# Optimization experiments

Hardware: AMD Instinct MI355X
Metric: run time of the kernel (lower is better)

## Reference

```python
import jax, jax.numpy as jnp
from jax import lax
import numpy as np

B, N, WID = 4096, 16, 64


def setup_inputs() -> dict:
    key = jax.random.key(0)
    ks = jax.random.split(key, 10)
    def nrm(k, shape, fan):
        return (jax.random.normal(k, shape) / np.float32(np.sqrt(fan))).astype(jnp.float32)
    x = 2.0 * jax.random.randint(ks[0], (B, N, N), 0, 2).astype(jnp.float32) - 1.0  # spins +/-1
    return {
        "x": x,
        "Wx": nrm(ks[1], (1, 2), 2),          # intermediate_x: Linear(2,1,bias=False)
        "Wh": nrm(ks[2], (WID, 2 * WID), 2 * WID),   # intermediate_h
        "Wh2": nrm(ks[3], (WID, 2 * WID), 2 * WID),  # intermediate_h2
        "Wih": nrm(ks[4], (4 * WID, 2), 2),   # LSTMCell weight_ih
        "Whh": nrm(ks[5], (4 * WID, WID), WID),  # LSTMCell weight_hh
        "bih": nrm(ks[6], (4 * WID,), WID),
        "bhh": nrm(ks[7], (4 * WID,), WID),
        "Wfc": nrm(ks[8], (2, WID), WID),     # fc1
        "bfc": nrm(ks[9], (2,), WID),
    }


def _log_prob(x, Wx, Wh, Wh2, Wih, Whh, bih, bhh, Wfc, bfc):
    Bn, n, _ = x.shape
    Wd = Whh.shape[1]
    dt = x.dtype

    # zigzag traversal: even rows left->right, odd rows right->left.
    # perm maps traversal position t -> column index; involutive (identity or reversal).
    perms = jnp.stack([jnp.arange(n) if i % 2 == 0 else jnp.arange(n)[::-1]
                       for i in range(n)])  # [n, n]
    x_rows = jnp.transpose(x, (1, 0, 2))                                  # [n, B, n]
    x_up_rows = jnp.concatenate([jnp.zeros((1, Bn, n), dt), x_rows[:-1]], 0)  # [n, B, n]

    Wh_p, Wh_u = Wh[:, :Wd], Wh[:, Wd:]
    Wh2_p, Wh2_u = Wh2[:, :Wd], Wh2[:, Wd:]

    def cell(carry, xs):
        h_prev, c_prev = carry          # [B, W] each (in-row previous cell, zeros at row start)
        x_prev, x_up, h_up, c_up = xs   # [B], [B], [B,W], [B,W]
        # slot 1 = previous cell along traversal, slot 2 = cell above
        x_inter = x_prev * Wx[0, 0] + x_up * Wx[0, 1]                     # [B]
        h_inter = h_prev @ Wh_p.T + h_up @ Wh_u.T                          # [B, W]
        c_inter = c_prev @ Wh2_p.T + c_up @ Wh2_u.T                        # [B, W]
        xh = (x_inter + 1.0) * 0.5
        emb = jnp.stack([xh, 1.0 - xh], axis=-1)                           # [B, 2]
        gates = emb @ Wih.T + bih + h_inter @ Whh.T + bhh                  # [B, 4W]
        ig, fg, gg, og = jnp.split(gates, 4, axis=-1)
        c_new = jax.nn.sigmoid(fg) * c_inter + jax.nn.sigmoid(ig) * jnp.tanh(gg)
        h_new = jax.nn.sigmoid(og) * jnp.tanh(c_new)
        y = jax.nn.log_softmax(h_new @ Wfc.T + bfc, axis=-1)               # [B, 2]
        return (h_new, c_new), (h_new, c_new, y)

    def row_step(carry, xs):
        h_row, c_row = carry            # [B, n, W] states of previous row (column order)
        x_row, x_up_row, perm = xs
        x_trav = x_row[:, perm]                                            # [B, n]
        x_prev_trav = jnp.concatenate([jnp.zeros((Bn, 1), dt), x_trav[:, :-1]], 1)
        x_up_trav = x_up_row[:, perm]
        h_up_trav = jnp.transpose(h_row[:, perm], (1, 0, 2))               # [n, B, W]
        c_up_trav = jnp.transpose(c_row[:, perm], (1, 0, 2))
        init = (jnp.zeros((Bn, Wd), dt), jnp.zeros((Bn, Wd), dt))
        _, (h_t, c_t, y_t) = lax.scan(
            cell, init, (x_prev_trav.T, x_up_trav.T, h_up_trav, c_up_trav))
        # traversal order -> column order (perm is its own inverse)
        h_col = jnp.transpose(h_t[perm], (1, 0, 2))                        # [B, n, W]
        c_col = jnp.transpose(c_t[perm], (1, 0, 2))
        y_col = y_t[perm]                                                  # [n, B, 2]
        return (h_col, c_col), y_col

    init = (jnp.zeros((Bn, n, Wd), dt), jnp.zeros((Bn, n, Wd), dt))
    _, ys = lax.scan(row_step, init, (x_rows, x_up_rows, perms))           # [n, n, B, 2]
    y = jnp.transpose(ys, (2, 0, 1, 3))                                    # [B, n, n, 2]

    mask = (1.0 + x) * 0.5
    lp = y[..., 0] * mask + y[..., 1] * (1.0 - mask)                       # [B, n, n]
    # final correction: samples with exactly one up spin
    aa = mask.sum((1, 2))
    rec = aa == 1
    jc = 0 if n % 2 == 0 else n - 1  # last visited cell of the zigzag
    factor = jnp.where(rec, 1.0 - mask[:, n - 1, jc], jnp.ones((), dt))
    lp = lp.at[:, n - 1, jc].multiply(factor)
    return lp.sum((1, 2))


def reference(x, Wx, Wh, Wh2, Wih, Whh, bih, bhh, Wfc, bfc):
    return _log_prob(x, Wx, Wh, Wh2, Wih, Whh, bih, bhh, Wfc, bfc)
```

## Files before the change

### kernel.cpp

```cpp
#include <hip/hip_runtime.h>

typedef __bf16 bf16x8 __attribute__((ext_vector_type(8)));
typedef float f32x4 __attribute__((ext_vector_type(4)));

#define MFMA(a,b,c) __builtin_amdgcn_mfma_f32_16x16x32_bf16((a),(b),(c),0,0,0)

__device__ __forceinline__ float rcp_(float x){ return __builtin_amdgcn_rcpf(x); }

__global__ __launch_bounds__(256) void prep_kernel(
    const float* __restrict__ Wh,  const float* __restrict__ Wh2,
    const float* __restrict__ Whh, const float* __restrict__ Wfc,
    __bf16* __restrict__ tbl)
{
  const int idx = blockIdx.x*256 + threadIdx.x;
  if (idx >= 256*176) return;
  const int e = idx & 7, f = (idx >> 3) % 22, t = idx / 176;
  const int w = t >> 6, lane = t & 63, l16 = lane & 15, g8 = (lane >> 4) * 8;
  float val;
  if (f < 16){
    const int g = (f >> 1) & 3, s = f & 1, half = f >> 3;
    const int n = g*64 + w*16 + l16;
    const int k = s*32 + g8 + e;
    const float* whcol = Wh + half*64 + k;
    float acc = 0.f;
    for (int j=0; j<64; ++j) acc += Whh[n*64 + j] * whcol[j*128];
    val = (g == 2) ? 2.f*acc : acc;
  } else if (f < 20){
    const int s = f - 16;
    const int n = w*16 + l16;
    const int k = s*32 + g8 + e;
    val = Wh2[n*128 + k];
  } else {
    const int s = f - 20;
    const int k = s*32 + g8 + e;
    val = Wfc[k] - Wfc[64 + k];
  }
  tbl[t*176 + f*8 + e] = (__bf16)val;
}

__global__ __launch_bounds__(256,1) void lstm2d_kernel(
    const float* __restrict__ x,   const float* __restrict__ Wx,
    const float* __restrict__ Wih,
    const float* __restrict__ bih, const float* __restrict__ bhh,
    const float* __restrict__ bfc,
    const __bf16* __restrict__ tbl,
    float* __restrict__ out)
{
  __shared__ __align__(16) __bf16 s_h[16*16*64];
  __shared__ __align__(16) __bf16 s_c[16*16*64];
  __shared__ __align__(16) float  s_xh[256*16];
  __shared__ unsigned int s_msk[16*8];

  const int tid  = threadIdx.x;
  const int w    = tid >> 6;
  const int lane = tid & 63;
  const int l16  = lane & 15;
  const int g4   = lane >> 4;
  const int g8   = g4 * 8;

  const float wx0 = Wx[0], wx1 = Wx[1];

  unsigned int* zh = (unsigned int*)s_h;
  unsigned int* zc = (unsigned int*)s_c;
  #pragma unroll
  for (int it=0; it<32; ++it){ zh[tid + it*256] = 0u; zc[tid + it*256] = 0u; }

  const float* xg = x + blockIdx.x * 4096;
  #pragma unroll
  for (int k=0; k<16; ++k){
    const int idx = tid + k*256;
    const int row = idx & 15, slot = idx >> 4;
    const int i = slot >> 4, t = slot & 15;
    const int c   = (i & 1) ? 15 - t : t;
    const int cpc = (i & 1) ? c + 1 : c - 1;
    const float xp = (t > 0) ? xg[row*256 + i*16 + cpc] : 0.f;
    const float xu = (i > 0) ? xg[row*256 + (i-1)*16 + c] : 0.f;
    s_xh[slot*16 + row] = (xp*wx0 + xu*wx1 + 1.f) * 0.5f;
  }
  if (tid < 128){
    const int row = tid >> 3, wd = tid & 7;
    unsigned int m = 0;
    for (int b=0; b<32; ++b){
      const int slot = wd*32 + b, i = slot >> 4, t = slot & 15;
      const int c = (i & 1) ? 15 - t : t;
      if (xg[row*256 + i*16 + c] > 0.f) m |= (1u << b);
    }
    s_msk[row*8 + wd] = m;
  }

  const __bf16* tb = tbl + tid*176;
  bf16x8 G1f[4][2], G2f[4][2], bcf[4], fcB[2];
  #pragma unroll
  for (int g=0; g<4; ++g)
    #pragma unroll
    for (int s=0; s<2; ++s){
      G1f[g][s] = *(const bf16x8*)(tb + (g*2+s)*8);
      G2f[g][s] = *(const bf16x8*)(tb + 64 + (g*2+s)*8);
    }
  #pragma unroll
  for (int s=0; s<4; ++s) bcf[s] = *(const bf16x8*)(tb + 128 + s*8);
  #pragma unroll
  for (int s=0; s<2; ++s) fcB[s] = *(const bf16x8*)(tb + 160 + s*8);

  const float bd = bfc[0] - bfc[1];
  float base_[4], dvec_[4];
  #pragma unroll
  for (int g=0; g<4; ++g){
    const int cg = g*64 + w*16 + l16;
    const float sc = (g == 2) ? 2.f : 1.f;
    base_[g] = (bih[cg] + bhh[cg] + Wih[cg*2+1]) * sc;
    dvec_[g] = (Wih[cg*2+0] - Wih[cg*2+1]) * sc;
  }
  const int colw = w*16 + l16;

  const int offA0 = l16*64 + ((     g8) ^ ((l16 & 7) << 3));
  const int offA1 = l16*64 + ((32 + g8) ^ ((l16 & 7) << 3));
  int stW[4];
  #pragma unroll
  for (int r=0;r<4;++r){
    const int row = g4*4 + r;
    stW[r] = row*64 + (colw ^ ((row & 7) << 3));
  }

  float lp[4] = {0.f,0.f,0.f,0.f};
  int   aa[4] = {0,0,0,0};

  __syncthreads();

  f32x4 accGu[4], aCu, aFp;

  for (int i=0; i<16; ++i){
    const int dir = i & 1;
    const int slot0 = i*16;

    {
      const int b = (dir ? 15 : 0) << 10;
      bf16x8 ah0 = *(const bf16x8*)(s_h + b + offA0);
      bf16x8 ah1 = *(const bf16x8*)(s_h + b + offA1);
      bf16x8 qc0 = *(const bf16x8*)(s_c + b + offA0);
      bf16x8 qc1 = *(const bf16x8*)(s_c + b + offA1);
      const float4 xh4 = *(const float4*)(s_xh + slot0*16 + g4*4);
      #pragma unroll
      for (int g=0; g<4; ++g){
        accGu[g][0] = base_[g] + xh4.x * dvec_[g];
        accGu[g][1] = base_[g] + xh4.y * dvec_[g];
        accGu[g][2] = base_[g] + xh4.z * dvec_[g];
        accGu[g][3] = base_[g] + xh4.w * dvec_[g];
        accGu[g] = MFMA(ah0, G2f[g][0], accGu[g]);
        accGu[g] = MFMA(ah1, G2f[g][1], accGu[g]);
      }
      f32x4 z = {0.f,0.f,0.f,0.f};
      aCu = MFMA(qc0, bcf[2], z);
      aCu = MFMA(qc1, bcf[3], aCu);
      f32x4 fz = {bd,bd,bd,bd};
      fz = MFMA(ah0, fcB[0], fz);
      aFp = MFMA(ah1, fcB[1], fz);
    }

    for (int t=0; t<16; ++t){
      const int c    = dir ? 15 - t : t;
      const int slot = slot0 + t;

      f32x4 accG[4], aC, aF;
      if (t > 0){
        const int b = (dir ? c + 1 : c - 1) << 10;
        bf16x8 a0 = *(const bf16x8*)(s_h + b + offA0);
        bf16x8 a1 = *(const bf16x8*)(s_h + b + offA1);
        bf16x8 q0 = *(const bf16x8*)(s_c + b + offA0);
        bf16x8 q1 = *(const bf16x8*)(s_c + b + offA1);
        #pragma unroll
        for (int g=0; g<4; ++g){
          accG[g] = MFMA(a0, G1f[g][0], accGu[g]);
          accG[g] = MFMA(a1, G1f[g][1], accG[g]);
        }
        aC = MFMA(q0, bcf[0], aCu);
        aC = MFMA(q1, bcf[1], aC);
        f32x4 fz = {bd,bd,bd,bd};
        fz = MFMA(a0, fcB[0], fz);
        aF = MFMA(a1, fcB[1], fz);
      } else {
        #pragma unroll
        for (int g=0; g<4; ++g) accG[g] = accGu[g];
        aC = aCu; aF = aFp;
      }

      if (slot > 0){
        const int ps = slot - 1;
        #pragma unroll
        for (int r=0;r<4;++r){
          const int msk = (s_msk[(g4*4+r)*8 + (ps >> 5)] >> (ps & 31)) & 1;
          const float d = aF[r];
          const float zz = msk ? -d : d;
          lp[r] -= __logf(1.f + __expf(zz));
          aa[r] += msk;
        }
      }

      if (t < 15){
        const int bu = (dir ? 14 - t : t + 1) << 10;
        bf16x8 au0 = *(const bf16x8*)(s_h + bu + offA0);
        bf16x8 au1 = *(const bf16x8*)(s_h + bu + offA1);
        bf16x8 cu0 = *(const bf16x8*)(s_c + bu + offA0);
        bf16x8 cu1 = *(const bf16x8*)(s_c + bu + offA1);
        const float4 xh4 = *(const float4*)(s_xh + (slot+1)*16 + g4*4);
        #pragma unroll
        for (int g=0; g<4; ++g){
          accGu[g][0] = base_[g] + xh4.x * dvec_[g];
          accGu[g][1] = base_[g] + xh4.y * dvec_[g];
          accGu[g][2] = base_[g] + xh4.z * dvec_[g];
          accGu[g][3] = base_[g] + xh4.w * dvec_[g];
          accGu[g] = MFMA(au0, G2f[g][0], accGu[g]);
          accGu[g] = MFMA(au1, G2f[g][1], accGu[g]);
        }
        f32x4 z = {0.f,0.f,0.f,0.f};
        aCu = MFMA(cu0, bcf[2], z);
        aCu = MFMA(cu1, bcf[3], aCu);
      }

      const int cb = c << 10;
      #pragma unroll
      for (int r=0;r<4;++r){
        const float ig = accG[0][r], fg = accG[1][r], gg = accG[2][r], og = accG[3][r];
        const float si = rcp_(1.f + __expf(-ig));
        const float sf = rcp_(1.f + __expf(-fg));
        const float tg = 2.f * rcp_(1.f + __expf(-gg)) - 1.f;
        const float cn = sf * aC[r] + si * tg;
        const float so = rcp_(1.f + __expf(-og));
        const float tc = 2.f * rcp_(1.f + __expf(-2.f*cn)) - 1.f;
        const float hn = so * tc;
        s_h[cb + stW[r]] = (__bf16)hn;
        s_c[cb + stW[r]] = (__bf16)cn;
      }

      __syncthreads();
    }
  }

  {
    bf16x8 a0 = *(const bf16x8*)(s_h + offA0);
    bf16x8 a1 = *(const bf16x8*)(s_h + offA1);
    f32x4 fz = {bd,bd,bd,bd};
    fz = MFMA(a0, fcB[0], fz);
    f32x4 aF = MFMA(a1, fcB[1], fz);
    #pragma unroll
    for (int r=0;r<4;++r){
      const int msk = (s_msk[(g4*4+r)*8 + 7] >> 31) & 1;
      const float d = aF[r];
      const float zz = msk ? -d : d;
      const float contrib = -__logf(1.f + __expf(zz));
      lp[r] += contrib; aa[r] += msk;
      if (aa[r] == 1 && msk) lp[r] -= contrib;
    }
    if (w == 0 && l16 == 0){
      #pragma unroll
      for (int r=0;r<4;++r) out[blockIdx.x*16 + g4*4 + r] = lp[r];
    }
  }
}

extern "C" void kernel_launch(void* const* d_in, const int* in_sizes, int n_in,
                              void* d_out, int out_size, void* d_ws, size_t ws_size,
                              hipStream_t stream) {
  const float* x   = (const float*)d_in[0];
  const float* Wx  = (const float*)d_in[1];
  const float* Wh  = (const float*)d_in[2];
  const float* Wh2 = (const float*)d_in[3];
  const float* Wih = (const float*)d_in[4];
  const float* Whh = (const float*)d_in[5];
  const float* bih = (const float*)d_in[6];
  const float* bhh = (const float*)d_in[7];
  const float* Wfc = (const float*)d_in[8];
  const float* bfc = (const float*)d_in[9];
  float* out = (float*)d_out;
  __bf16* tbl = (__bf16*)d_ws;

  prep_kernel<<<dim3(176), dim3(256), 0, stream>>>(Wh, Wh2, Whh, Wfc, tbl);
  lstm2d_kernel<<<dim3(256), dim3(256), 0, stream>>>(
      x, Wx, Wih, bih, bhh, bfc, tbl, out);
}
```

Baseline: 258.5 us.

## Split LSTM gate work across 8 waves with shuffle exchange and deferred log-prob

Doubles the block to 512 threads so each wave owns 8 hidden columns and computes two gate tiles (half the MFMAs per wave), exchanging gate values between lane halves via shuffles. Folds the log2(e) scaling into the weight tables so exp2f replaces expf, and moves bias/input-weight constants into the prep table. The fc1 logit is computed only by wave 0 and stored to shared memory, and the log-sigmoid reduction is deferred to a parallel pass after the recurrence instead of running every step. The cost is more waves synchronizing at each of the 256 barriers, plus shuffle overhead and an extra reduction phase.

```diff
diff --git a/kernel.cpp b/kernel.cpp
--- a/kernel.cpp
+++ b/kernel.cpp
@@ -6,50 +6,69 @@
 #define MFMA(a,b,c) __builtin_amdgcn_mfma_f32_16x16x32_bf16((a),(b),(c),0,0,0)
 
 __device__ __forceinline__ float rcp_(float x){ return __builtin_amdgcn_rcpf(x); }
+
+#define L2E 1.4426950408889634f
+#define LN2 0.6931471805599453f
 
 __global__ __launch_bounds__(256) void prep_kernel(
     const float* __restrict__ Wh,  const float* __restrict__ Wh2,
     const float* __restrict__ Whh, const float* __restrict__ Wfc,
-    __bf16* __restrict__ tbl)
+    const float* __restrict__ Wih, const float* __restrict__ bih,
+    const float* __restrict__ bhh,
+    char* __restrict__ tblc)
 {
   const int idx = blockIdx.x*256 + threadIdx.x;
-  if (idx >= 256*176) return;
-  const int e = idx & 7, f = (idx >> 3) % 22, t = idx / 176;
-  const int w = t >> 6, lane = t & 63, l16 = lane & 15, g8 = (lane >> 4) * 8;
-  float val;
-  if (f < 16){
-    const int g = (f >> 1) & 3, s = f & 1, half = f >> 3;
-    const int n = g*64 + w*16 + l16;
-    const int k = s*32 + g8 + e;
-    const float* whcol = Wh + half*64 + k;
-    float acc = 0.f;
-    for (int j=0; j<64; ++j) acc += Whh[n*64 + j] * whcol[j*128];
-    val = (g == 2) ? 2.f*acc : acc;
-  } else if (f < 20){
-    const int s = f - 16;
-    const int n = w*16 + l16;
-    const int k = s*32 + g8 + e;
-    val = Wh2[n*128 + k];
-  } else {
-    const int s = f - 20;
-    const int k = s*32 + g8 + e;
-    val = Wfc[k] - Wfc[64 + k];
-  }
-  tbl[t*176 + f*8 + e] = (__bf16)val;
+  if (idx < 512*14*8){
+    const int e = idx & 7, f = (idx >> 3) % 14, t = (idx >> 3) / 14;
+    const int w = t >> 6, lane = t & 63, l16 = lane & 15;
+    const int g8 = ((lane >> 4) & 3) * 8;
+    const int hcol = w*8 + (l16 & 7), hi = l16 >> 3;
+    float val;
+    if (f < 8){
+      const int half = (f >> 2) & 1;
+      const int tile = (f >> 1) & 1;
+      const int s    = f & 1;
+      const int gate = tile*2 + hi;
+      const int n = gate*64 + hcol;
+      const int k = s*32 + g8 + e;
+      float acc = 0.f;
+      for (int j=0; j<64; ++j) acc += Whh[n*64 + j] * Wh[j*128 + half*64 + k];
+      val = acc * ((gate == 2) ? 2.f*L2E : L2E);
+    } else if (f < 12){
+      const int s = f - 8;
+      const int k = (s & 1)*32 + g8 + e;
+      val = Wh2[hcol*128 + (s >> 1)*64 + k];
+    } else {
+      const int k = (f & 1)*32 + g8 + e;
+      val = Wfc[k] - Wfc[64 + k];
+    }
+    *(__bf16*)(tblc + t*240 + f*16 + e*2) = (__bf16)val;
+  } else if (idx < 512*14*8 + 512*4){
+    const int j = idx - 512*14*8;
+    const int t = j >> 2, q = j & 3;
+    const int w = t >> 6, lane = t & 63, l16 = lane & 15, hi = l16 >> 3;
+    const int tile = q >> 1, kind = q & 1;
+    const int gate = tile*2 + hi;
+    const int n = gate*64 + w*8 + (l16 & 7);
+    const float sc = (gate == 2) ? 2.f*L2E : L2E;
+    const float v = kind ? sc*(Wih[n*2] - Wih[n*2+1])
+                         : sc*(bih[n] + bhh[n] + Wih[n*2+1]);
+    *(float*)(tblc + t*240 + 224 + q*4) = v;
+  }
 }
 
-__global__ __launch_bounds__(256,1) void lstm2d_kernel(
+__global__ __launch_bounds__(512,2) void lstm2d_kernel(
     const float* __restrict__ x,   const float* __restrict__ Wx,
-    const float* __restrict__ Wih,
-    const float* __restrict__ bih, const float* __restrict__ bhh,
     const float* __restrict__ bfc,
-    const __bf16* __restrict__ tbl,
+    const char* __restrict__ tblc,
     float* __restrict__ out)
 {
   __shared__ __align__(16) __bf16 s_h[16*16*64];
   __shared__ __align__(16) __bf16 s_c[16*16*64];
   __shared__ __align__(16) float  s_xh[256*16];
+  __shared__ __align__(16) float  s_d[256*16];
   __shared__ unsigned int s_msk[16*8];
+  __shared__ float s_red[8*16];
 
   const int tid  = threadIdx.x;
   const int w    = tid >> 6;
@@ -57,18 +76,21 @@
   const int l16  = lane & 15;
   const int g4   = lane >> 4;
   const int g8   = g4 * 8;
+  const int hi   = l16 >> 3;
+  const bool lo  = (hi == 0);
 
   const float wx0 = Wx[0], wx1 = Wx[1];
+  const float bd  = bfc[0] - bfc[1];
 
   unsigned int* zh = (unsigned int*)s_h;
   unsigned int* zc = (unsigned int*)s_c;
   #pragma unroll
-  for (int it=0; it<32; ++it){ zh[tid + it*256] = 0u; zc[tid + it*256] = 0u; }
+  for (int it=0; it<16; ++it){ zh[tid + it*512] = 0u; zc[tid + it*512] = 0u; }
 
   const float* xg = x + blockIdx.x * 4096;
   #pragma unroll
-  for (int k=0; k<16; ++k){
-    const int idx = tid + k*256;
+  for (int k=0; k<8; ++k){
+    const int idx = tid + k*512;
     const int row = idx & 15, slot = idx >> 4;
     const int i = slot >> 4, t = slot & 15;
     const int c   = (i & 1) ? 15 - t : t;
@@ -88,173 +110,183 @@
     s_msk[row*8 + wd] = m;
   }
 
-  const __bf16* tb = tbl + tid*176;
-  bf16x8 G1f[4][2], G2f[4][2], bcf[4], fcB[2];
+  const char* tb = tblc + tid*240;
+  bf16x8 g1T0[2], g1T1[2], g2T0[2], g2T1[2], cB[4], fcB[2];
+  g1T0[0] = *(const bf16x8*)(tb +   0); g1T0[1] = *(const bf16x8*)(tb +  16);
+  g1T1[0] = *(const bf16x8*)(tb +  32); g1T1[1] = *(const bf16x8*)(tb +  48);
+  g2T0[0] = *(const bf16x8*)(tb +  64); g2T0[1] = *(const bf16x8*)(tb +  80);
+  g2T1[0] = *(const bf16x8*)(tb +  96); g2T1[1] = *(const bf16x8*)(tb + 112);
   #pragma unroll
-  for (int g=0; g<4; ++g)
-    #pragma unroll
-    for (int s=0; s<2; ++s){
-      G1f[g][s] = *(const bf16x8*)(tb + (g*2+s)*8);
-      G2f[g][s] = *(const bf16x8*)(tb + 64 + (g*2+s)*8);
-    }
-  #pragma unroll
-  for (int s=0; s<4; ++s) bcf[s] = *(const bf16x8*)(tb + 128 + s*8);
-  #pragma unroll
-  for (int s=0; s<2; ++s) fcB[s] = *(const bf16x8*)(tb + 160 + s*8);
-
-  const float bd = bfc[0] - bfc[1];
-  float base_[4], dvec_[4];
-  #pragma unroll
-  for (int g=0; g<4; ++g){
-    const int cg = g*64 + w*16 + l16;
-    const float sc = (g == 2) ? 2.f : 1.f;
-    base_[g] = (bih[cg] + bhh[cg] + Wih[cg*2+1]) * sc;
-    dvec_[g] = (Wih[cg*2+0] - Wih[cg*2+1]) * sc;
-  }
-  const int colw = w*16 + l16;
+  for (int s=0; s<4; ++s) cB[s] = *(const bf16x8*)(tb + 128 + s*16);
+  fcB[0] = *(const bf16x8*)(tb + 192); fcB[1] = *(const bf16x8*)(tb + 208);
+  const float base0 = *(const float*)(tb + 224);
+  const float dvec0 = *(const float*)(tb + 228);
+  const float base1 = *(const float*)(tb + 232);
+  const float dvec1 = *(const float*)(tb + 236);
 
   const int offA0 = l16*64 + ((     g8) ^ ((l16 & 7) << 3));
   const int offA1 = l16*64 + ((32 + g8) ^ ((l16 & 7) << 3));
-  int stW[4];
+  const int habs = w*8 + (l16 & 7);
+  int stWa[2];
   #pragma unroll
-  for (int r=0;r<4;++r){
-    const int row = g4*4 + r;
-    stW[r] = row*64 + (colw ^ ((row & 7) << 3));
-  }
-
-  float lp[4] = {0.f,0.f,0.f,0.f};
-  int   aa[4] = {0,0,0,0};
+  for (int e=0; e<2; ++e){
+    const int R = g4*4 + 2*hi + e;
+    stWa[e] = R*64 + (habs ^ ((R & 7) << 3));
+  }
+  const float C2 = -2.f*L2E;
 
   __syncthreads();
 
-  f32x4 accGu[4], aCu, aFp;
+  f32x4 aT0u, aT1u, aCu;
 
   for (int i=0; i<16; ++i){
     const int dir = i & 1;
     const int slot0 = i*16;
 
     {
-      const int b = (dir ? 15 : 0) << 10;
-      bf16x8 ah0 = *(const bf16x8*)(s_h + b + offA0);
-      bf16x8 ah1 = *(const bf16x8*)(s_h + b + offA1);
-      bf16x8 qc0 = *(const bf16x8*)(s_c + b + offA0);
-      bf16x8 qc1 = *(const bf16x8*)(s_c + b + offA1);
+      const int bu = (dir ? 15 : 0) << 10;
+      bf16x8 h0 = *(const bf16x8*)(s_h + bu + offA0);
+      bf16x8 h1 = *(const bf16x8*)(s_h + bu + offA1);
+      bf16x8 c0 = *(const bf16x8*)(s_c + bu + offA0);
+      bf16x8 c1 = *(const bf16x8*)(s_c + bu + offA1);
       const float4 xh4 = *(const float4*)(s_xh + slot0*16 + g4*4);
       #pragma unroll
-      for (int g=0; g<4; ++g){
-        accGu[g][0] = base_[g] + xh4.x * dvec_[g];
-        accGu[g][1] = base_[g] + xh4.y * dvec_[g];
-        accGu[g][2] = base_[g] + xh4.z * dvec_[g];
-        accGu[g][3] = base_[g] + xh4.w * dvec_[g];
-        accGu[g] = MFMA(ah0, G2f[g][0], accGu[g]);
-        accGu[g] = MFMA(ah1, G2f[g][1], accGu[g]);
-      }
+      for (int r=0;r<4;++r){
+        const float xh = (&xh4.x)[r];
+        aT0u[r] = base0 + xh*dvec0;
+        aT1u[r] = base1 + xh*dvec1;
+      }
+      aT0u = MFMA(h0, g2T0[0], aT0u); aT0u = MFMA(h1, g2T0[1], aT0u);
+      aT1u = MFMA(h0, g2T1[0], aT1u); aT1u = MFMA(h1, g2T1[1], aT1u);
       f32x4 z = {0.f,0.f,0.f,0.f};
-      aCu = MFMA(qc0, bcf[2], z);
-      aCu = MFMA(qc1, bcf[3], aCu);
-      f32x4 fz = {bd,bd,bd,bd};
-      fz = MFMA(ah0, fcB[0], fz);
-      aFp = MFMA(ah1, fcB[1], fz);
+      aCu = MFMA(c0, cB[2], z); aCu = MFMA(c1, cB[3], aCu);
+      if (w == 0 && i > 0){
+        f32x4 fz = {bd,bd,bd,bd};
+        fz = MFMA(h0, fcB[0], fz);
+        f32x4 aF = MFMA(h1, fcB[1], fz);
+        if (l16 == 0){
+          #pragma unroll
+          for (int r=0;r<4;++r) s_d[(slot0-1)*16 + g4*4 + r] = aF[r];
+        }
+      }
     }
 
     for (int t=0; t<16; ++t){
       const int c    = dir ? 15 - t : t;
       const int slot = slot0 + t;
 
-      f32x4 accG[4], aC, aF;
+      f32x4 aT0 = aT0u, aT1 = aT1u, aC = aCu;
       if (t > 0){
-        const int b = (dir ? c + 1 : c - 1) << 10;
-        bf16x8 a0 = *(const bf16x8*)(s_h + b + offA0);
-        bf16x8 a1 = *(const bf16x8*)(s_h + b + offA1);
-        bf16x8 q0 = *(const bf16x8*)(s_c + b + offA0);
-        bf16x8 q1 = *(const bf16x8*)(s_c + b + offA1);
-        #pragma unroll
-        for (int g=0; g<4; ++g){
-          accG[g] = MFMA(a0, G1f[g][0], accGu[g]);
-          accG[g] = MFMA(a1, G1f[g][1], accG[g]);
+        const int bp = (dir ? c + 1 : c - 1) << 10;
+        bf16x8 a0 = *(const bf16x8*)(s_h + bp + offA0);
+        bf16x8 a1 = *(const bf16x8*)(s_h + bp + offA1);
+        bf16x8 q0 = *(const bf16x8*)(s_c + bp + offA0);
+        bf16x8 q1 = *(const bf16x8*)(s_c + bp + offA1);
+        aT0 = MFMA(a0, g1T0[0], aT0); aT0 = MFMA(a1, g1T0[1], aT0);
+        aT1 = MFMA(a0, g1T1[0], aT1); aT1 = MFMA(a1, g1T1[1], aT1);
+        aC  = MFMA(q0, cB[0], aC);    aC  = MFMA(q1, cB[1], aC);
+        if (w == 0){
+          f32x4 fz = {bd,bd,bd,bd};
+          fz = MFMA(a0, fcB[0], fz);
+          f32x4 aF = MFMA(a1, fcB[1], fz);
+          if (l16 == 0){
+            #pragma unroll
+            for (int r=0;r<4;++r) s_d[(slot-1)*16 + g4*4 + r] = aF[r];
+          }
         }
-        aC = MFMA(q0, bcf[0], aCu);
-        aC = MFMA(q1, bcf[1], aC);
-        f32x4 fz = {bd,bd,bd,bd};
-        fz = MFMA(a0, fcB[0], fz);
-        aF = MFMA(a1, fcB[1], fz);
-      } else {
-        #pragma unroll
-        for (int g=0; g<4; ++g) accG[g] = accGu[g];
-        aC = aCu; aF = aFp;
-      }
-
-      if (slot > 0){
-        const int ps = slot - 1;
+      }
+
+      if (t < 15){
+        const int bu = (dir ? 14 - t : t + 1) << 10;
+        bf16x8 h0 = *(const bf16x8*)(s_h + bu + offA0);
+        bf16x8 h1 = *(const bf16x8*)(s_h + bu + offA1);
+        bf16x8 c0 = *(const bf16x8*)(s_c + bu + offA0);
+        bf16x8 c1 = *(const bf16x8*)(s_c + bu + offA1);
+        const float4 xh4 = *(const float4*)(s_xh + (slot+1)*16 + g4*4);
         #pragma unroll
         for (int r=0;r<4;++r){
-          const int msk = (s_msk[(g4*4+r)*8 + (ps >> 5)] >> (ps & 31)) & 1;
-          const float d = aF[r];
-          const float zz = msk ? -d : d;
-          lp[r] -= __logf(1.f + __expf(zz));
-          aa[r] += msk;
+          const float xh = (&xh4.x)[r];
+          aT0u[r] = base0 + xh*dvec0;
+          aT1u[r] = base1 + xh*dvec1;
         }
-      }
-
-      if (t < 15){
-        const int bu = (dir ? 14 - t : t + 1) << 10;
-        bf16x8 au0 = *(const bf16x8*)(s_h + bu + offA0);
-        bf16x8 au1 = *(const bf16x8*)(s_h + bu + offA1);
-        bf16x8 cu0 = *(const bf16x8*)(s_c + bu + offA0);
-        bf16x8 cu1 = *(const bf16x8*)(s_c + bu + offA1);
-        const float4 xh4 = *(const float4*)(s_xh + (slot+1)*16 + g4*4);
-        #pragma unroll
-        for (int g=0; g<4; ++g){
-          accGu[g][0] = base_[g] + xh4.x * dvec_[g];
-          accGu[g][1] = base_[g] + xh4.y * dvec_[g];
-          accGu[g][2] = base_[g] + xh4.z * dvec_[g];
-          accGu[g][3] = base_[g] + xh4.w * dvec_[g];
-          accGu[g] = MFMA(au0, G2f[g][0], accGu[g]);
-          accGu[g] = MFMA(au1, G2f[g][1], accGu[g]);
-        }
+        aT0u = MFMA(h0, g2T0[0], aT0u); aT0u = MFMA(h1, g2T0[1], aT0u);
+        aT1u = MFMA(h0, g2T1[0], aT1u); aT1u = MFMA(h1, g2T1[1], aT1u);
         f32x4 z = {0.f,0.f,0.f,0.f};
-        aCu = MFMA(cu0, bcf[2], z);
-        aCu = MFMA(cu1, bcf[3], aCu);
+        aCu = MFMA(c0, cB[2], z); aCu = MFMA(c1, cB[3], aCu);
       }
 
       const int cb = c << 10;
       #pragma unroll
-      for (int r=0;r<4;++r){
-        const float ig = accG[0][r], fg = accG[1][r], gg = accG[2][r], og = accG[3][r];
-        const float si = rcp_(1.f + __expf(-ig));
-        const float sf = rcp_(1.f + __expf(-fg));
-        const float tg = 2.f * rcp_(1.f + __expf(-gg)) - 1.f;
-        const float cn = sf * aC[r] + si * tg;
-        const float so = rcp_(1.f + __expf(-og));
-        const float tc = 2.f * rcp_(1.f + __expf(-2.f*cn)) - 1.f;
+      for (int e=0; e<2; ++e){
+        const float sendT0 = lo ? aT0[2+e] : aT0[e];
+        const float sendT1 = lo ? aT1[2+e] : aT1[e];
+        const float rT0 = __shfl_xor(sendT0, 8);
+        const float rT1 = __shfl_xor(sendT1, 8);
+        const float own0 = lo ? aT0[e] : aT0[2+e];
+        const float own1 = lo ? aT1[e] : aT1[2+e];
+        const float ig = lo ? own0 : rT0;
+        const float fg = lo ? rT0  : own0;
+        const float gg = lo ? own1 : rT1;
+        const float og = lo ? rT1  : own1;
+        const float cI = lo ? aC[e] : aC[2+e];
+        const float si = rcp_(1.f + exp2f(-ig));
+        const float sf = rcp_(1.f + exp2f(-fg));
+        const float tg = 2.f * rcp_(1.f + exp2f(-gg)) - 1.f;
+        const float cn = sf*cI + si*tg;
+        const float so = rcp_(1.f + exp2f(-og));
+        const float tc = 2.f * rcp_(1.f + exp2f(C2*cn)) - 1.f;
         const float hn = so * tc;
-        s_h[cb + stW[r]] = (__bf16)hn;
-        s_c[cb + stW[r]] = (__bf16)cn;
+        s_h[cb + stWa[e]] = (__bf16)hn;
+        s_c[cb + stWa[e]] = (__bf16)cn;
       }
 
       __syncthreads();
     }
   }
 
-  {
+  if (w == 0){
     bf16x8 a0 = *(const bf16x8*)(s_h + offA0);
     bf16x8 a1 = *(const bf16x8*)(s_h + offA1);
     f32x4 fz = {bd,bd,bd,bd};
     fz = MFMA(a0, fcB[0], fz);
     f32x4 aF = MFMA(a1, fcB[1], fz);
+    if (l16 == 0){
+      #pragma unroll
+      for (int r=0;r<4;++r) s_d[255*16 + g4*4 + r] = aF[r];
+    }
+  }
+  __syncthreads();
+
+  {
+    const int row = tid & 15, grp = tid >> 4;
+    float lpp = 0.f;
     #pragma unroll
-    for (int r=0;r<4;++r){
-      const int msk = (s_msk[(g4*4+r)*8 + 7] >> 31) & 1;
-      const float d = aF[r];
+    for (int e=0; e<8; ++e){
+      const int slot = grp*8 + e;
+      const float d = s_d[slot*16 + row];
+      const int msk = (s_msk[row*8 + (slot >> 5)] >> (slot & 31)) & 1;
       const float zz = msk ? -d : d;
-      const float contrib = -__logf(1.f + __expf(zz));
-      lp[r] += contrib; aa[r] += msk;
-      if (aa[r] == 1 && msk) lp[r] -= contrib;
-    }
-    if (w == 0 && l16 == 0){
-      #pragma unroll
-      for (int r=0;r<4;++r) out[blockIdx.x*16 + g4*4 + r] = lp[r];
-    }
+      lpp -= LN2 * log2f(1.f + exp2f(zz * L2E));
+    }
+    lpp += __shfl_xor(lpp, 16);
+    lpp += __shfl_xor(lpp, 32);
+    if (lane < 16) s_red[w*16 + lane] = lpp;
+  }
+  __syncthreads();
+  if (tid < 16){
+    const int row = tid;
+    float lp = 0.f;
+    #pragma unroll
+    for (int ww=0; ww<8; ++ww) lp += s_red[ww*16 + row];
+    int aa = 0;
+    #pragma unroll
+    for (int wd=0; wd<8; ++wd) aa += __popc(s_msk[row*8 + wd]);
+    const int m255 = (s_msk[row*8 + 7] >> 31) & 1;
+    if (aa == 1 && m255){
+      const float d = s_d[255*16 + row];
+      lp += LN2 * log2f(1.f + exp2f(-d * L2E));
+    }
+    out[blockIdx.x*16 + row] = lp;
   }
 }
 
@@ -272,9 +304,9 @@
   const float* Wfc = (const float*)d_in[8];
   const float* bfc = (const float*)d_in[9];
   float* out = (float*)d_out;
-  __bf16* tbl = (__bf16*)d_ws;
-
-  prep_kernel<<<dim3(176), dim3(256), 0, stream>>>(Wh, Wh2, Whh, Wfc, tbl);
-  lstm2d_kernel<<<dim3(256), dim3(256), 0, stream>>>(
-      x, Wx, Wih, bih, bhh, bfc, tbl, out);
+  char* tbl = (char*)d_ws;
+
+  prep_kernel<<<dim3(((512*14*8 + 512*4) + 255)/256), dim3(256), 0, stream>>>(
+      Wh, Wh2, Whh, Wfc, Wih, bih, bhh, tbl);
+  lstm2d_kernel<<<dim3(256), dim3(512), 0, stream>>>(x, Wx, bfc, tbl, out);
 }
```

Result: slower. 274.4 us (+6.1%).

## Halve samples per block to 8 and defer log-prob reduction to epilogue

Applied to the files above, without the earlier changes.

Each block now handles 8 samples instead of 16, so the grid doubles to 512 blocks and spreads work over more compute units on the serial 256-step recurrence. The MFMA M-dimension is still 16, so half the rows are duplicated and only lanes with g4<2 store results, which wastes half of each MFMA. The fc logit is computed by a single rotating wave per step and stored to shared memory. The softplus log-prob accumulation moves out of the recurrent loop into a parallel reduction at the end.

```diff
diff --git a/kernel.cpp b/kernel.cpp
--- a/kernel.cpp
+++ b/kernel.cpp
@@ -46,10 +46,12 @@
     const __bf16* __restrict__ tbl,
     float* __restrict__ out)
 {
-  __shared__ __align__(16) __bf16 s_h[16*16*64];
-  __shared__ __align__(16) __bf16 s_c[16*16*64];
-  __shared__ __align__(16) float  s_xh[256*16];
-  __shared__ unsigned int s_msk[16*8];
+  __shared__ __align__(16) __bf16 s_h[16*8*64];
+  __shared__ __align__(16) __bf16 s_c[16*8*64];
+  __shared__ __align__(16) float  s_xh[256*8];
+  __shared__ __align__(16) float  s_d[256*8];
+  __shared__ unsigned int s_msk[8*8];
+  __shared__ float s_red[32];
 
   const int tid  = threadIdx.x;
   const int w    = tid >> 6;
@@ -57,27 +59,29 @@
   const int l16  = lane & 15;
   const int g4   = lane >> 4;
   const int g8   = g4 * 8;
+  const int rl   = l16 & 7;
+  const bool vld = (g4 < 2);
 
   const float wx0 = Wx[0], wx1 = Wx[1];
 
   unsigned int* zh = (unsigned int*)s_h;
   unsigned int* zc = (unsigned int*)s_c;
   #pragma unroll
-  for (int it=0; it<32; ++it){ zh[tid + it*256] = 0u; zc[tid + it*256] = 0u; }
-
-  const float* xg = x + blockIdx.x * 4096;
-  #pragma unroll
-  for (int k=0; k<16; ++k){
+  for (int it=0; it<16; ++it){ zh[tid + it*256] = 0u; zc[tid + it*256] = 0u; }
+
+  const float* xg = x + blockIdx.x * 2048;
+  #pragma unroll
+  for (int k=0; k<8; ++k){
     const int idx = tid + k*256;
-    const int row = idx & 15, slot = idx >> 4;
+    const int row = idx & 7, slot = idx >> 3;
     const int i = slot >> 4, t = slot & 15;
     const int c   = (i & 1) ? 15 - t : t;
     const int cpc = (i & 1) ? c + 1 : c - 1;
     const float xp = (t > 0) ? xg[row*256 + i*16 + cpc] : 0.f;
     const float xu = (i > 0) ? xg[row*256 + (i-1)*16 + c] : 0.f;
-    s_xh[slot*16 + row] = (xp*wx0 + xu*wx1 + 1.f) * 0.5f;
-  }
-  if (tid < 128){
+    s_xh[slot*8 + row] = (xp*wx0 + xu*wx1 + 1.f) * 0.5f;
+  }
+  if (tid < 64){
     const int row = tid >> 3, wd = tid & 7;
     unsigned int m = 0;
     for (int b=0; b<32; ++b){
@@ -113,33 +117,31 @@
   }
   const int colw = w*16 + l16;
 
-  const int offA0 = l16*64 + ((     g8) ^ ((l16 & 7) << 3));
-  const int offA1 = l16*64 + ((32 + g8) ^ ((l16 & 7) << 3));
+  const int offA0 = rl*64 + ((     g8) ^ (rl << 3));
+  const int offA1 = rl*64 + ((32 + g8) ^ (rl << 3));
   int stW[4];
   #pragma unroll
   for (int r=0;r<4;++r){
-    const int row = g4*4 + r;
-    stW[r] = row*64 + (colw ^ ((row & 7) << 3));
-  }
-
-  float lp[4] = {0.f,0.f,0.f,0.f};
-  int   aa[4] = {0,0,0,0};
+    const int R = (g4 & 1)*4 + r;
+    stW[r] = R*64 + (colw ^ (R << 3));
+  }
+  const int xhOff = (g4 & 1) * 4;
 
   __syncthreads();
 
-  f32x4 accGu[4], aCu, aFp;
+  f32x4 accGu[4], aCu;
 
   for (int i=0; i<16; ++i){
     const int dir = i & 1;
     const int slot0 = i*16;
 
     {
-      const int b = (dir ? 15 : 0) << 10;
+      const int b = (dir ? 15 : 0) << 9;
       bf16x8 ah0 = *(const bf16x8*)(s_h + b + offA0);
       bf16x8 ah1 = *(const bf16x8*)(s_h + b + offA1);
       bf16x8 qc0 = *(const bf16x8*)(s_c + b + offA0);
       bf16x8 qc1 = *(const bf16x8*)(s_c + b + offA1);
-      const float4 xh4 = *(const float4*)(s_xh + slot0*16 + g4*4);
+      const float4 xh4 = *(const float4*)(s_xh + slot0*8 + xhOff);
       #pragma unroll
       for (int g=0; g<4; ++g){
         accGu[g][0] = base_[g] + xh4.x * dvec_[g];
@@ -152,18 +154,24 @@
       f32x4 z = {0.f,0.f,0.f,0.f};
       aCu = MFMA(qc0, bcf[2], z);
       aCu = MFMA(qc1, bcf[3], aCu);
-      f32x4 fz = {bd,bd,bd,bd};
-      fz = MFMA(ah0, fcB[0], fz);
-      aFp = MFMA(ah1, fcB[1], fz);
+      if (i > 0 && w == 3){
+        f32x4 fz = {bd,bd,bd,bd};
+        fz = MFMA(ah0, fcB[0], fz);
+        f32x4 aF = MFMA(ah1, fcB[1], fz);
+        if (l16 == 0 && vld){
+          #pragma unroll
+          for (int r=0;r<4;++r) s_d[(slot0-1)*8 + (g4&1)*4 + r] = aF[r];
+        }
+      }
     }
 
     for (int t=0; t<16; ++t){
       const int c    = dir ? 15 - t : t;
       const int slot = slot0 + t;
 
-      f32x4 accG[4], aC, aF;
+      f32x4 accG[4], aC;
       if (t > 0){
-        const int b = (dir ? c + 1 : c - 1) << 10;
+        const int b = (dir ? c + 1 : c - 1) << 9;
         bf16x8 a0 = *(const bf16x8*)(s_h + b + offA0);
         bf16x8 a1 = *(const bf16x8*)(s_h + b + offA1);
         bf16x8 q0 = *(const bf16x8*)(s_c + b + offA0);
@@ -175,34 +183,28 @@
         }
         aC = MFMA(q0, bcf[0], aCu);
         aC = MFMA(q1, bcf[1], aC);
-        f32x4 fz = {bd,bd,bd,bd};
-        fz = MFMA(a0, fcB[0], fz);
-        aF = MFMA(a1, fcB[1], fz);
+        if (w == ((t - 1) & 3)){
+          f32x4 fz = {bd,bd,bd,bd};
+          fz = MFMA(a0, fcB[0], fz);
+          f32x4 aF = MFMA(a1, fcB[1], fz);
+          if (l16 == 0 && vld){
+            #pragma unroll
+            for (int r=0;r<4;++r) s_d[(slot-1)*8 + (g4&1)*4 + r] = aF[r];
+          }
+        }
       } else {
         #pragma unroll
         for (int g=0; g<4; ++g) accG[g] = accGu[g];
-        aC = aCu; aF = aFp;
-      }
-
-      if (slot > 0){
-        const int ps = slot - 1;
-        #pragma unroll
-        for (int r=0;r<4;++r){
-          const int msk = (s_msk[(g4*4+r)*8 + (ps >> 5)] >> (ps & 31)) & 1;
-          const float d = aF[r];
-          const float zz = msk ? -d : d;
-          lp[r] -= __logf(1.f + __expf(zz));
-          aa[r] += msk;
-        }
+        aC = aCu;
       }
 
       if (t < 15){
-        const int bu = (dir ? 14 - t : t + 1) << 10;
+        const int bu = (dir ? 14 - t : t + 1) << 9;
         bf16x8 au0 = *(const bf16x8*)(s_h + bu + offA0);
         bf16x8 au1 = *(const bf16x8*)(s_h + bu + offA1);
         bf16x8 cu0 = *(const bf16x8*)(s_c + bu + offA0);
         bf16x8 cu1 = *(const bf16x8*)(s_c + bu + offA1);
-        const float4 xh4 = *(const float4*)(s_xh + (slot+1)*16 + g4*4);
+        const float4 xh4 = *(const float4*)(s_xh + (slot+1)*8 + xhOff);
         #pragma unroll
         for (int g=0; g<4; ++g){
           accGu[g][0] = base_[g] + xh4.x * dvec_[g];
@@ -217,44 +219,71 @@
         aCu = MFMA(cu1, bcf[3], aCu);
       }
 
-      const int cb = c << 10;
-      #pragma unroll
-      for (int r=0;r<4;++r){
-        const float ig = accG[0][r], fg = accG[1][r], gg = accG[2][r], og = accG[3][r];
-        const float si = rcp_(1.f + __expf(-ig));
-        const float sf = rcp_(1.f + __expf(-fg));
-        const float tg = 2.f * rcp_(1.f + __expf(-gg)) - 1.f;
-        const float cn = sf * aC[r] + si * tg;
-        const float so = rcp_(1.f + __expf(-og));
-        const float tc = 2.f * rcp_(1.f + __expf(-2.f*cn)) - 1.f;
-        const float hn = so * tc;
-        s_h[cb + stW[r]] = (__bf16)hn;
-        s_c[cb + stW[r]] = (__bf16)cn;
+      if (vld){
+        const int cb = c << 9;
+        #pragma unroll
+        for (int r=0;r<4;++r){
+          const float ig = accG[0][r], fg = accG[1][r], gg = accG[2][r], og = accG[3][r];
+          const float si = rcp_(1.f + __expf(-ig));
+          const float sf = rcp_(1.f + __expf(-fg));
+          const float tg = 2.f * rcp_(1.f + __expf(-gg)) - 1.f;
+          const float cn = sf * aC[r] + si * tg;
+          const float so = rcp_(1.f + __expf(-og));
+          const float tc = 2.f * rcp_(1.f + __expf(-2.f*cn)) - 1.f;
+          const float hn = so * tc;
+          s_h[cb + stW[r]] = (__bf16)hn;
+          s_c[cb + stW[r]] = (__bf16)cn;
+        }
       }
 
       __syncthreads();
     }
   }
 
-  {
+  if (w == 3){
     bf16x8 a0 = *(const bf16x8*)(s_h + offA0);
     bf16x8 a1 = *(const bf16x8*)(s_h + offA1);
     f32x4 fz = {bd,bd,bd,bd};
     fz = MFMA(a0, fcB[0], fz);
     f32x4 aF = MFMA(a1, fcB[1], fz);
+    if (l16 == 0 && vld){
+      #pragma unroll
+      for (int r=0;r<4;++r) s_d[255*8 + (g4&1)*4 + r] = aF[r];
+    }
+  }
+  __syncthreads();
+
+  {
+    const int row = lane & 7, grpw = lane >> 3;
+    float lpp = 0.f;
     #pragma unroll
-    for (int r=0;r<4;++r){
-      const int msk = (s_msk[(g4*4+r)*8 + 7] >> 31) & 1;
-      const float d = aF[r];
+    for (int e=0; e<8; ++e){
+      const int slot = (w*8 + grpw)*8 + e;
+      const float d = s_d[slot*8 + row];
+      const int msk = (s_msk[row*8 + (slot >> 5)] >> (slot & 31)) & 1;
       const float zz = msk ? -d : d;
-      const float contrib = -__logf(1.f + __expf(zz));
-      lp[r] += contrib; aa[r] += msk;
-      if (aa[r] == 1 && msk) lp[r] -= contrib;
-    }
-    if (w == 0 && l16 == 0){
-      #pragma unroll
-      for (int r=0;r<4;++r) out[blockIdx.x*16 + g4*4 + r] = lp[r];
-    }
+      lpp -= __logf(1.f + __expf(zz));
+    }
+    lpp += __shfl_xor(lpp, 8);
+    lpp += __shfl_xor(lpp, 16);
+    lpp += __shfl_xor(lpp, 32);
+    if (lane < 8) s_red[w*8 + lane] = lpp;
+  }
+  __syncthreads();
+  if (tid < 8){
+    const int row = tid;
+    float lp = 0.f;
+    #pragma unroll
+    for (int ww=0; ww<4; ++ww) lp += s_red[ww*8 + row];
+    int aa = 0;
+    #pragma unroll
+    for (int wd=0; wd<8; ++wd) aa += __popc(s_msk[row*8 + wd]);
+    const int m255 = (s_msk[row*8 + 7] >> 31) & 1;
+    if (aa == 1 && m255){
+      const float d = s_d[255*8 + row];
+      lp += __logf(1.f + __expf(-d));
+    }
+    out[blockIdx.x*8 + row] = lp;
   }
 }
 
@@ -275,6 +304,6 @@
   __bf16* tbl = (__bf16*)d_ws;
 
   prep_kernel<<<dim3(176), dim3(256), 0, stream>>>(Wh, Wh2, Whh, Wfc, tbl);
-  lstm2d_kernel<<<dim3(256), dim3(256), 0, stream>>>(
+  lstm2d_kernel<<<dim3(512), dim3(256), 0, stream>>>(
       x, Wx, Wih, bih, bhh, bfc, tbl, out);
 }
```

Measured after the change: 300.7 us. +16.3%, slower.

## Defer log-prob to an epilogue, round-robin fc1 across waves, fold log2e into weights

Applied to the files above, without the earlier changes.

The fc1 projection is now computed by a single wave per step, chosen round-robin. The per-slot logit is stored in shared memory, and all softplus log-prob terms plus the up-spin count are evaluated in a parallel epilogue after the recurrence. This takes them off the serial per-cell critical path. The gate weights and biases are prescaled by log2(e) so the LSTM activations use exp2. The sigmoid/tanh combination is also rewritten to share reciprocals, cutting the transcendental count per cell. The cost is extra LDS (s_d, s_red) and a final reduction pass.

```diff
diff --git a/kernel.cpp b/kernel.cpp
--- a/kernel.cpp
+++ b/kernel.cpp
@@ -6,6 +6,8 @@
 #define MFMA(a,b,c) __builtin_amdgcn_mfma_f32_16x16x32_bf16((a),(b),(c),0,0,0)
 
 __device__ __forceinline__ float rcp_(float x){ return __builtin_amdgcn_rcpf(x); }
+
+#define L2E 1.4426950408889634f
 
 __global__ __launch_bounds__(256) void prep_kernel(
     const float* __restrict__ Wh,  const float* __restrict__ Wh2,
@@ -24,7 +26,7 @@
     const float* whcol = Wh + half*64 + k;
     float acc = 0.f;
     for (int j=0; j<64; ++j) acc += Whh[n*64 + j] * whcol[j*128];
-    val = (g == 2) ? 2.f*acc : acc;
+    val = acc * ((g == 2) ? 2.f*L2E : L2E);
   } else if (f < 20){
     const int s = f - 16;
     const int n = w*16 + l16;
@@ -49,7 +51,9 @@
   __shared__ __align__(16) __bf16 s_h[16*16*64];
   __shared__ __align__(16) __bf16 s_c[16*16*64];
   __shared__ __align__(16) float  s_xh[256*16];
+  __shared__ __align__(16) float  s_d[256*16];
   __shared__ unsigned int s_msk[16*8];
+  __shared__ float s_red[256];
 
   const int tid  = threadIdx.x;
   const int w    = tid >> 6;
@@ -107,7 +111,7 @@
   #pragma unroll
   for (int g=0; g<4; ++g){
     const int cg = g*64 + w*16 + l16;
-    const float sc = (g == 2) ? 2.f : 1.f;
+    const float sc = (g == 2) ? 2.f*L2E : L2E;
     base_[g] = (bih[cg] + bhh[cg] + Wih[cg*2+1]) * sc;
     dvec_[g] = (Wih[cg*2+0] - Wih[cg*2+1]) * sc;
   }
@@ -121,13 +125,11 @@
     const int row = g4*4 + r;
     stW[r] = row*64 + (colw ^ ((row & 7) << 3));
   }
-
-  float lp[4] = {0.f,0.f,0.f,0.f};
-  int   aa[4] = {0,0,0,0};
+  const float C2 = -2.f*L2E;
 
   __syncthreads();
 
-  f32x4 accGu[4], aCu, aFp;
+  f32x4 accGu[4], aCu;
 
   for (int i=0; i<16; ++i){
     const int dir = i & 1;
@@ -152,16 +154,22 @@
       f32x4 z = {0.f,0.f,0.f,0.f};
       aCu = MFMA(qc0, bcf[2], z);
       aCu = MFMA(qc1, bcf[3], aCu);
-      f32x4 fz = {bd,bd,bd,bd};
-      fz = MFMA(ah0, fcB[0], fz);
-      aFp = MFMA(ah1, fcB[1], fz);
+      if (i > 0 && w == 3){
+        f32x4 fz = {bd,bd,bd,bd};
+        fz = MFMA(ah0, fcB[0], fz);
+        f32x4 aF = MFMA(ah1, fcB[1], fz);
+        if (l16 == 0){
+          #pragma unroll
+          for (int r=0;r<4;++r) s_d[(slot0-1)*16 + g4*4 + r] = aF[r];
+        }
+      }
     }
 
     for (int t=0; t<16; ++t){
       const int c    = dir ? 15 - t : t;
       const int slot = slot0 + t;
 
-      f32x4 accG[4], aC, aF;
+      f32x4 accG[4], aC;
       if (t > 0){
         const int b = (dir ? c + 1 : c - 1) << 10;
         bf16x8 a0 = *(const bf16x8*)(s_h + b + offA0);
@@ -175,25 +183,19 @@
         }
         aC = MFMA(q0, bcf[0], aCu);
         aC = MFMA(q1, bcf[1], aC);
-        f32x4 fz = {bd,bd,bd,bd};
-        fz = MFMA(a0, fcB[0], fz);
-        aF = MFMA(a1, fcB[1], fz);
+        if (w == ((t - 1) & 3)){
+          f32x4 fz = {bd,bd,bd,bd};
+          fz = MFMA(a0, fcB[0], fz);
+          f32x4 aF = MFMA(a1, fcB[1], fz);
+          if (l16 == 0){
+            #pragma unroll
+            for (int r=0;r<4;++r) s_d[(slot-1)*16 + g4*4 + r] = aF[r];
+          }
+        }
       } else {
         #pragma unroll
         for (int g=0; g<4; ++g) accG[g] = accGu[g];
-        aC = aCu; aF = aFp;
-      }
-
-      if (slot > 0){
-        const int ps = slot - 1;
-        #pragma unroll
-        for (int r=0;r<4;++r){
-          const int msk = (s_msk[(g4*4+r)*8 + (ps >> 5)] >> (ps & 31)) & 1;
-          const float d = aF[r];
-          const float zz = msk ? -d : d;
-          lp[r] -= __logf(1.f + __expf(zz));
-          aa[r] += msk;
-        }
+        aC = aCu;
       }
 
       if (t < 15){
@@ -217,44 +219,70 @@
         aCu = MFMA(cu1, bcf[3], aCu);
       }
 
-      const int cb = c << 10;
-      #pragma unroll
-      for (int r=0;r<4;++r){
-        const float ig = accG[0][r], fg = accG[1][r], gg = accG[2][r], og = accG[3][r];
-        const float si = rcp_(1.f + __expf(-ig));
-        const float sf = rcp_(1.f + __expf(-fg));
-        const float tg = 2.f * rcp_(1.f + __expf(-gg)) - 1.f;
-        const float cn = sf * aC[r] + si * tg;
-        const float so = rcp_(1.f + __expf(-og));
-        const float tc = 2.f * rcp_(1.f + __expf(-2.f*cn)) - 1.f;
-        const float hn = so * tc;
-        s_h[cb + stW[r]] = (__bf16)hn;
-        s_c[cb + stW[r]] = (__bf16)cn;
+      {
+        const int cb = c << 10;
+        #pragma unroll
+        for (int r=0;r<4;++r){
+          const float A = exp2f(-accG[0][r]);
+          const float F = exp2f(-accG[1][r]);
+          const float B = exp2f(-accG[2][r]);
+          const float O = exp2f(-accG[3][r]);
+          const float a1 = 1.f + A, f1 = 1.f + F, b1 = 1.f + B, o1 = 1.f + O;
+          const float pab = a1 * b1;
+          const float num = fmaf(1.f - B, f1, aC[r] * pab);
+          const float cn  = num * rcp_(pab * f1);
+          const float E   = exp2f(C2 * cn);
+          const float hn  = (1.f - E) * rcp_(o1 * (1.f + E));
+          s_h[cb + stW[r]] = (__bf16)hn;
+          s_c[cb + stW[r]] = (__bf16)cn;
+        }
       }
 
       __syncthreads();
     }
   }
 
-  {
+  if (w == 3){
     bf16x8 a0 = *(const bf16x8*)(s_h + offA0);
     bf16x8 a1 = *(const bf16x8*)(s_h + offA1);
     f32x4 fz = {bd,bd,bd,bd};
     fz = MFMA(a0, fcB[0], fz);
     f32x4 aF = MFMA(a1, fcB[1], fz);
+    if (l16 == 0){
+      #pragma unroll
+      for (int r=0;r<4;++r) s_d[255*16 + g4*4 + r] = aF[r];
+    }
+  }
+  __syncthreads();
+
+  {
+    const int row = tid & 15, grp = tid >> 4;
+    float lpp = 0.f;
     #pragma unroll
-    for (int r=0;r<4;++r){
-      const int msk = (s_msk[(g4*4+r)*8 + 7] >> 31) & 1;
-      const float d = aF[r];
+    for (int e=0; e<16; ++e){
+      const int slot = grp*16 + e;
+      const float d = s_d[slot*16 + row];
+      const int msk = (s_msk[row*8 + (slot >> 5)] >> (slot & 31)) & 1;
       const float zz = msk ? -d : d;
-      const float contrib = -__logf(1.f + __expf(zz));
-      lp[r] += contrib; aa[r] += msk;
-      if (aa[r] == 1 && msk) lp[r] -= contrib;
-    }
-    if (w == 0 && l16 == 0){
-      #pragma unroll
-      for (int r=0;r<4;++r) out[blockIdx.x*16 + g4*4 + r] = lp[r];
-    }
+      lpp -= __logf(1.f + __expf(zz));
+    }
+    s_red[grp*16 + row] = lpp;
+  }
+  __syncthreads();
+  if (tid < 16){
+    const int row = tid;
+    float lp = 0.f;
+    #pragma unroll
+    for (int g=0; g<16; ++g) lp += s_red[g*16 + row];
+    int aa = 0;
+    #pragma unroll
+    for (int wd=0; wd<8; ++wd) aa += __popc(s_msk[row*8 + wd]);
+    const int m255 = (s_msk[row*8 + 7] >> 31) & 1;
+    if (aa == 1 && m255){
+      const float d = s_d[255*16 + row];
+      lp += __logf(1.f + __expf(-d));
+    }
+    out[blockIdx.x*16 + row] = lp;
   }
 }
 
```

After: 249.1 us. 3.6% less time.
